# Performance work log

Hardware: AMD Instinct MI355X
Metric: run time of the kernel (lower is better)

Reference implementation:

```python
import jax, jax.numpy as jnp
import numpy as np

N_HEADS = 16

def setup_inputs() -> dict:
    key = jax.random.key(0)
    k1, k2, k3 = jax.random.split(key, 3)
    B, S, V = 4, 2048, 1024
    hs = V // N_HEADS
    x = jax.random.normal(k1, (B, S, V), dtype=jnp.float32)
    # per-head shared QKV projection: Linear(head_size, 3*head_size), weight [3*hs, hs]
    W_qkv = jax.random.normal(k2, (3 * hs, hs), dtype=jnp.float32) / np.sqrt(hs)
    W_out = jax.random.normal(k3, (V, V), dtype=jnp.float32) / np.sqrt(V)
    return {"x": x, "W_qkv": W_qkv, "W_out": W_out}

def reference(x, W_qkv, W_out):
    B, S, V = x.shape
    hs = V // N_HEADS
    x_head = x.reshape(B, S, N_HEADS, hs)            # [B,S,H,hs]
    qkv = jnp.einsum('bshd,ed->bshe', x_head, W_qkv)  # [B,S,H,3*hs]
    q, k, v = jnp.split(qkv, 3, axis=-1)
    scale = 1.0 / np.sqrt(hs).astype(np.float32)
    scores = jnp.einsum('bqhd,bkhd->bhqk', q, k) * scale  # [B,H,S,S]
    causal = jnp.tril(jnp.ones((S, S), dtype=bool))       # keep j <= i
    scores = jnp.where(causal, scores, -jnp.inf)
    attn = jax.nn.softmax(scores, axis=-1)                # dropout p=0 (eval)
    o = jnp.einsum('bhqk,bkhd->bqhd', attn, v).reshape(B, S, V)
    return o @ W_out.T
```

## Files before the change

kernel.cpp:

```cpp
#include <hip/hip_runtime.h>

#define B_  4
#define S_  2048
#define V_  1024
#define H_  16
#define HS_ 64
#define GK_ 1024
#define GN_ 1024

typedef unsigned short u16;
typedef __bf16 bf16x8 __attribute__((ext_vector_type(8)));
typedef float  f32x4  __attribute__((ext_vector_type(4)));

__device__ __forceinline__ float bf2f(u16 u) {
  return __uint_as_float(((unsigned int)u) << 16);
}
__device__ __forceinline__ float lo16(unsigned int w) { return __uint_as_float(w << 16); }
__device__ __forceinline__ float hi16(unsigned int w) { return __uint_as_float(w & 0xffff0000u); }
__device__ __forceinline__ u16 f2bf(float f) {
  unsigned int u = __float_as_uint(f);
  unsigned int r = u + 0x7fffu + ((u >> 16) & 1u);
  return (u16)(r >> 16);
}

__global__ __launch_bounds__(256) void detect_kernel(
    const unsigned int* __restrict__ x32, int* __restrict__ flag)
{
  __shared__ int zred[256];
  __shared__ int nred[256];
  const int tid = threadIdx.x;
  int nz = 0, nn = 0;
  for (int i = tid; i < 16384; i += 256) {
    unsigned int lo = x32[i] & 0xffffu;
    if (lo == 0u) nz++;
    if ((lo & 0x7f80u) == 0x7f80u && (lo & 0x7fu) != 0u) nn++;
  }
  zred[tid] = nz; nred[tid] = nn;
  __syncthreads();
  for (int s = 128; s > 0; s >>= 1) {
    if (tid < s) { zred[tid] += zred[tid + s]; nred[tid] += nred[tid + s]; }
    __syncthreads();
  }
  if (tid == 0) *flag = (zred[0] > 8192 || nred[0] > 0) ? 1 : 0;
}

__global__ __launch_bounds__(256) void wcvt_kernel(
    const void* __restrict__ w, u16* __restrict__ wb, const int* __restrict__ flag)
{
  const int i = (blockIdx.x * 256 + threadIdx.x) * 4;
  if (*flag) {
    float4 f = *(const float4*)((const float*)w + i);
    unsigned int p0 = (unsigned int)f2bf(f.x) | ((unsigned int)f2bf(f.y) << 16);
    unsigned int p1 = (unsigned int)f2bf(f.z) | ((unsigned int)f2bf(f.w) << 16);
    *(uint2*)(wb + i) = make_uint2(p0, p1);
  } else {
    *(uint2*)(wb + i) = *(const uint2*)((const u16*)w + i);
  }
}

__global__ __launch_bounds__(256) void qkv_mfma_kernel(
    const void* __restrict__ x, const void* __restrict__ wqkv,
    u16* __restrict__ q, u16* __restrict__ k, u16* __restrict__ v,
    const int* __restrict__ flag)
{
  __shared__ __align__(16) u16 Ws[192 * 80];
  const int tid = threadIdx.x;
  const int isf32 = *flag;
  for (int idx = tid; idx < 192 * 4; idx += 256) {
    const int row = idx >> 2, c0 = (idx & 3) * 16;
    u16 t16[16];
    if (isf32) {
      const float* gp = (const float*)wqkv + row * 64 + c0;
#pragma unroll
      for (int e = 0; e < 16; ++e) t16[e] = f2bf(gp[e]);
    } else {
      const u16* gp = (const u16*)wqkv + row * 64 + c0;
      *(uint4*)t16 = *(const uint4*)gp;
      *(uint4*)(t16 + 8) = *(const uint4*)(gp + 8);
    }
    *(uint4*)(Ws + row * 80 + c0) = *(uint4*)t16;
    *(uint4*)(Ws + row * 80 + c0 + 8) = *(uint4*)(t16 + 8);
  }
  __syncthreads();

  const int m0 = blockIdx.x * 128;
  const int w = tid >> 6, lane = tid & 63;
  const int ar = lane & 15, quad = lane >> 4;
  const int rbase = m0 + (w & 1) * 64;
  const int cbase = (w >> 1) * 96;

  bf16x8 af[4][2];
#pragma unroll
  for (int rt = 0; rt < 4; ++rt) {
    const size_t row = (size_t)(rbase + rt * 16 + ar) * 64;
    if (isf32) {
      const float* gp = (const float*)x + row;
#pragma unroll
      for (int ks = 0; ks < 2; ++ks) {
        u16 t8[8];
        const float* g8 = gp + ks * 32 + quad * 8;
#pragma unroll
        for (int e = 0; e < 8; ++e) t8[e] = f2bf(g8[e]);
        af[rt][ks] = *(bf16x8*)t8;
      }
    } else {
      const u16* gp = (const u16*)x + row;
#pragma unroll
      for (int ks = 0; ks < 2; ++ks)
        af[rt][ks] = *(const bf16x8*)(gp + ks * 32 + quad * 8);
    }
  }

  f32x4 acc[4][6] = {};
#pragma unroll
  for (int ks = 0; ks < 2; ++ks)
#pragma unroll
    for (int t = 0; t < 6; ++t) {
      const bf16x8 bfr = *(const bf16x8*)(Ws + (cbase + t * 16 + ar) * 80 + ks * 32 + quad * 8);
#pragma unroll
      for (int rt = 0; rt < 4; ++rt)
        acc[rt][t] = __builtin_amdgcn_mfma_f32_16x16x32_bf16(af[rt][ks], bfr, acc[rt][t], 0, 0, 0);
    }

#pragma unroll
  for (int rt = 0; rt < 4; ++rt)
#pragma unroll
    for (int r = 0; r < 4; ++r) {
      const int m = rbase + rt * 16 + quad * 4 + r;
      const int z = m >> 15, s = (m >> 4) & (S_ - 1), h = m & (H_ - 1);
      const size_t base = (((size_t)z * H_ + h) * S_ + s) * HS_;
#pragma unroll
      for (int t = 0; t < 6; ++t) {
        const int e = cbase + t * 16 + ar;
        u16* dst = (e < 64) ? q : (e < 128) ? k : v;
        dst[base + (e & 63)] = f2bf(acc[rt][t][r]);
      }
    }
}

__global__ __launch_bounds__(256) void qkv_kernel(
    const void* __restrict__ x, int b0, const void* __restrict__ w,
    u16* __restrict__ q, u16* __restrict__ k, u16* __restrict__ v,
    const int* __restrict__ flag)
{
  __shared__ __align__(16) float Ws[192 * 64];
  const int tid = threadIdx.x;
  const int isf32 = *flag;
  if (isf32) {
    for (int i = tid; i < 192 * 64; i += 256) Ws[i] = ((const float*)w)[i];
  } else {
    for (int i = tid; i < 192 * 64; i += 256) Ws[i] = bf2f(((const u16*)w)[i]);
  }
  __syncthreads();

  const int th = blockIdx.x * 256 + tid;
  const int h = th & (H_ - 1);
  const int s = th >> 4;
  const int b = b0 + blockIdx.z;
  const size_t zoff = (size_t)blockIdx.z * H_ * S_ * HS_;
  const size_t xoff = ((size_t)b * S_ + s) * V_ + h * HS_;

  float xf[64];
  if (isf32) {
    const float4* xp = (const float4*)((const float*)x + xoff);
#pragma unroll
    for (int i = 0; i < 16; ++i) {
      float4 u = xp[i];
      xf[4*i+0] = u.x; xf[4*i+1] = u.y; xf[4*i+2] = u.z; xf[4*i+3] = u.w;
    }
  } else {
    const uint4* xp = (const uint4*)((const u16*)x + xoff);
#pragma unroll
    for (int i = 0; i < 8; ++i) {
      uint4 u = xp[i];
      xf[8*i+0] = lo16(u.x); xf[8*i+1] = hi16(u.x);
      xf[8*i+2] = lo16(u.y); xf[8*i+3] = hi16(u.y);
      xf[8*i+4] = lo16(u.z); xf[8*i+5] = hi16(u.z);
      xf[8*i+6] = lo16(u.w); xf[8*i+7] = hi16(u.w);
    }
  }

  const size_t obase = zoff + ((size_t)h * S_ + s) * HS_;
#pragma unroll 1
  for (int eg = 0; eg < 12; ++eg) {
    float acc[16];
#pragma unroll
    for (int ee = 0; ee < 16; ++ee) {
      const float4* wr = (const float4*)&Ws[(eg * 16 + ee) * 64];
      float a = 0.f;
#pragma unroll
      for (int d4 = 0; d4 < 16; ++d4) {
        float4 wv = wr[d4];
        a += xf[d4*4+0]*wv.x + xf[d4*4+1]*wv.y + xf[d4*4+2]*wv.z + xf[d4*4+3]*wv.w;
      }
      acc[ee] = a;
    }
    u16* dst = (eg < 4) ? q : (eg < 8) ? k : v;
    const int d0 = (eg & 3) * 16;
    unsigned int p[8];
#pragma unroll
    for (int t = 0; t < 8; ++t)
      p[t] = (unsigned int)f2bf(acc[2*t]) | ((unsigned int)f2bf(acc[2*t+1]) << 16);
    uint4* dp = (uint4*)(dst + obase + d0);
    dp[0] = make_uint4(p[0], p[1], p[2], p[3]);
    dp[1] = make_uint4(p[4], p[5], p[6], p[7]);
  }
}

__global__ __launch_bounds__(256, 4) void attn_mfma_kernel(
    const u16* __restrict__ q, const u16* __restrict__ k,
    const u16* __restrict__ v, u16* __restrict__ o)
{
  const int z   = blockIdx.z;
  const int h   = blockIdx.y;
  const int bi  = blockIdx.x;
  const int qb0 = bi * 64;
  const int qb1 = (31 - bi) * 64;
  const int tid = threadIdx.x;
  const int w = tid >> 6, lane = tid & 63;
  const int col = lane & 15, quad = lane >> 4;

  __shared__ __align__(16) u16 Ks[64 * 72];
  __shared__ __align__(16) u16 Vt[64 * 72];
  __shared__ __align__(16) u16 Ps[4][16 * 72];

  const size_t hs = ((size_t)z * H_ + h) * S_ * HS_;

  const float qs = 0.125f * 1.44269504089f;
  bf16x8 qf[2][2];
#pragma unroll
  for (int u = 0; u < 2; ++u) {
    const int qb = u ? qb1 : qb0;
    const u16* qp = q + hs + (size_t)(qb + w * 16 + col) * HS_ + quad * 8;
#pragma unroll
    for (int ks = 0; ks < 2; ++ks) {
      u16 t8[8];
      *(uint4*)t8 = *(const uint4*)(qp + ks * 32);
#pragma unroll
      for (int e = 0; e < 8; ++e) t8[e] = f2bf(bf2f(t8[e]) * qs);
      qf[u][ks] = *(bf16x8*)t8;
    }
  }

  const int sr = tid >> 2, sc = (tid & 3) * 16;
  const int vr = (tid & 31) * 2, vc = (tid >> 5) * 8;

  f32x4 oacc[2][4] = {};
  float m_run[2] = {-INFINITY, -INFINITY};
  float l_run[2] = {0.f, 0.f};

  const int jbmax = qb1;

  uint4 k0, k1, va, vb;
  {
    const u16* kp = k + hs + (size_t)sr * HS_ + sc;
    k0 = *(const uint4*)kp;
    k1 = *(const uint4*)(kp + 8);
    const u16* vp = v + hs + (size_t)vr * HS_ + vc;
    va = *(const uint4*)vp;
    vb = *(const uint4*)(vp + HS_);
  }

  for (int jb = 0; jb <= jbmax; jb += 64) {
    __syncthreads();
    *(uint4*)(Ks + sr * 72 + sc)     = k0;
    *(uint4*)(Ks + sr * 72 + sc + 8) = k1;
    {
      const u16* pa = (const u16*)&va;
      const u16* pb = (const u16*)&vb;
#pragma unroll
      for (int e = 0; e < 8; ++e)
        *(unsigned int*)(Vt + (vc + e) * 72 + vr) =
            (unsigned int)pa[e] | ((unsigned int)pb[e] << 16);
    }
    __syncthreads();

    if (jb < jbmax) {
      const u16* kp = k + hs + (size_t)(jb + 64 + sr) * HS_ + sc;
      k0 = *(const uint4*)kp;
      k1 = *(const uint4*)(kp + 8);
      const u16* vp = v + hs + (size_t)(jb + 64 + vr) * HS_ + vc;
      va = *(const uint4*)vp;
      vb = *(const uint4*)(vp + HS_);
    }

#pragma unroll
    for (int u = 0; u < 2; ++u) {
      const int ru = (u ? qb1 : qb0) + w * 16;
      if (jb > ru + 15) continue;

      f32x4 sacc[4] = {};
      __builtin_amdgcn_s_setprio(1);
#pragma unroll
      for (int ks = 0; ks < 2; ++ks)
#pragma unroll
        for (int t = 0; t < 4; ++t) {
          const bf16x8 kf = *(const bf16x8*)(Ks + (t * 16 + col) * 72 + ks * 32 + quad * 8);
          sacc[t] = __builtin_amdgcn_mfma_f32_16x16x32_bf16(kf, qf[u][ks], sacc[t], 0, 0, 0);
        }
      __builtin_amdgcn_s_setprio(0);

      if (jb + 63 > ru) {
        const int q_l = ru + col;
#pragma unroll
        for (int t = 0; t < 4; ++t) {
          const int kb = jb + t * 16 + quad * 4;
#pragma unroll
          for (int r = 0; r < 4; ++r)
            if (kb + r > q_l) sacc[t][r] = -INFINITY;
        }
      }

      float a0 = fmaxf(fmaxf(sacc[0][0], sacc[0][1]), fmaxf(sacc[0][2], sacc[0][3]));
      float a1 = fmaxf(fmaxf(sacc[1][0], sacc[1][1]), fmaxf(sacc[1][2], sacc[1][3]));
      float a2 = fmaxf(fmaxf(sacc[2][0], sacc[2][1]), fmaxf(sacc[2][2], sacc[2][3]));
      float a3 = fmaxf(fmaxf(sacc[3][0], sacc[3][1]), fmaxf(sacc[3][2], sacc[3][3]));
      float mx = fmaxf(fmaxf(a0, a1), fmaxf(a2, a3));
      mx = fmaxf(mx, __shfl_xor(mx, 16));
      mx = fmaxf(mx, __shfl_xor(mx, 32));

      float m = m_run[u];
      if (__any(mx - m > 8.0f)) {
        const float mn = fmaxf(m, mx);
        const float al = __builtin_amdgcn_exp2f(m - mn);
        m = mn; m_run[u] = mn;
        l_run[u] *= al;
        float alr[4];
#pragma unroll
        for (int r = 0; r < 4; ++r) alr[r] = __shfl(al, quad * 4 + r);
#pragma unroll
        for (int nt = 0; nt < 4; ++nt)
#pragma unroll
          for (int r = 0; r < 4; ++r) oacc[u][nt][r] *= alr[r];
      }

      float ls = 0.f;
#pragma unroll
      for (int t = 0; t < 4; ++t) {
        const float p0 = __builtin_amdgcn_exp2f(sacc[t][0] - m);
        const float p1 = __builtin_amdgcn_exp2f(sacc[t][1] - m);
        const float p2 = __builtin_amdgcn_exp2f(sacc[t][2] - m);
        const float p3 = __builtin_amdgcn_exp2f(sacc[t][3] - m);
        ls += (p0 + p1) + (p2 + p3);
        const unsigned int w0 = (unsigned int)f2bf(p0) | ((unsigned int)f2bf(p1) << 16);
        const unsigned int w1 = (unsigned int)f2bf(p2) | ((unsigned int)f2bf(p3) << 16);
        *(uint2*)(Ps[w] + col * 72 + t * 16 + quad * 4) = make_uint2(w0, w1);
      }
      ls += __shfl_xor(ls, 16);
      ls += __shfl_xor(ls, 32);
      l_run[u] += ls;

      __builtin_amdgcn_s_setprio(1);
#pragma unroll
      for (int ks = 0; ks < 2; ++ks) {
        const bf16x8 pf = *(const bf16x8*)(Ps[w] + col * 72 + ks * 32 + quad * 8);
#pragma unroll
        for (int nt = 0; nt < 4; ++nt) {
          const bf16x8 vf = *(const bf16x8*)(Vt + (nt * 16 + col) * 72 + ks * 32 + quad * 8);
          oacc[u][nt] = __builtin_amdgcn_mfma_f32_16x16x32_bf16(pf, vf, oacc[u][nt], 0, 0, 0);
        }
      }
      __builtin_amdgcn_s_setprio(0);
    }
  }

  u16* ob = o + (size_t)z * S_ * V_ + h * HS_;
#pragma unroll
  for (int u = 0; u < 2; ++u) {
    const int ru = (u ? qb1 : qb0) + w * 16;
    float inv[4];
#pragma unroll
    for (int r = 0; r < 4; ++r) inv[r] = 1.0f / __shfl(l_run[u], quad * 4 + r);
#pragma unroll
    for (int nt = 0; nt < 4; ++nt)
#pragma unroll
      for (int r = 0; r < 4; ++r)
        ob[(size_t)(ru + quad * 4 + r) * V_ + nt * 16 + col] = f2bf(oacc[u][nt][r] * inv[r]);
  }
}

__global__ __launch_bounds__(256) void oproj_mfma_kernel(
    const u16* __restrict__ a, const u16* __restrict__ bw, float* __restrict__ c)
{
  __shared__ __align__(16) u16 As[128 * 40];
  __shared__ __align__(16) u16 Bs[128 * 40];
  const int tid = threadIdx.x;
  const int m0 = blockIdx.x * 128;
  const int n0 = blockIdx.y * 128;
  const int w = tid >> 6, lane = tid & 63;
  const int col = lane & 15, quad = lane >> 4;
  const int qr = (w & 1) * 64;
  const int qc = (w >> 1) * 64;

  f32x4 acc[4][4] = {};

  const int sr = tid >> 2;
  const int sk = (tid & 3) * 8;
  const u16* ga = a  + (size_t)(m0 + sr) * GK_ + sk;
  const u16* gb = bw + (size_t)(n0 + sr) * GK_ + sk;

  for (int k0 = 0; k0 < GK_; k0 += 32) {
    uint4 a0 = *(const uint4*)(ga + k0);
    uint4 a1 = *(const uint4*)(ga + (size_t)64 * GK_ + k0);
    uint4 b0 = *(const uint4*)(gb + k0);
    uint4 b1 = *(const uint4*)(gb + (size_t)64 * GK_ + k0);
    __syncthreads();
    *(uint4*)(As + sr * 40 + sk)        = a0;
    *(uint4*)(As + (64 + sr) * 40 + sk) = a1;
    *(uint4*)(Bs + sr * 40 + sk)        = b0;
    *(uint4*)(Bs + (64 + sr) * 40 + sk) = b1;
    __syncthreads();

    bf16x8 af[4], bfr[4];
#pragma unroll
    for (int i = 0; i < 4; ++i) {
      af[i]  = *(const bf16x8*)(As + (qr + i * 16 + col) * 40 + quad * 8);
      bfr[i] = *(const bf16x8*)(Bs + (qc + i * 16 + col) * 40 + quad * 8);
    }
#pragma unroll
    for (int i = 0; i < 4; ++i)
#pragma unroll
      for (int j = 0; j < 4; ++j)
        acc[i][j] = __builtin_amdgcn_mfma_f32_16x16x32_bf16(af[i], bfr[j], acc[i][j], 0, 0, 0);
  }

#pragma unroll
  for (int i = 0; i < 4; ++i)
#pragma unroll
    for (int j = 0; j < 4; ++j)
#pragma unroll
      for (int r = 0; r < 4; ++r)
        c[(size_t)(m0 + qr + i * 16 + quad * 4 + r) * GN_ + n0 + qc + j * 16 + col]
            = acc[i][j][r];
}

__global__ __launch_bounds__(256) void oproj_vec_kernel(
    const u16* __restrict__ o, const void* __restrict__ w,
    float* __restrict__ out, const int* __restrict__ flag)
{
  __shared__ __align__(16) float At[64 * 68];
  __shared__ __align__(16) float Wt[64 * 68];
  const int tid = threadIdx.x;
  const size_t zo = (size_t)blockIdx.z * S_ * V_;
  const int m0 = blockIdx.x * 64;
  const int n0 = blockIdx.y * 64;
  const int tr = tid >> 4, tc = tid & 15;
  const int isf32 = *flag;
  const int srow = tid >> 2, sc = (tid & 3) * 16;

  float acc[4][4] = {};

  for (int k0 = 0; k0 < GK_; k0 += 64) {
    float av[16], wv[16];
    {
      const u16* gp = o + zo + (size_t)(m0 + srow) * GK_ + k0 + sc;
      uint4 u0 = *(const uint4*)gp;
      uint4 u1 = *(const uint4*)(gp + 8);
      av[0]=lo16(u0.x); av[1]=hi16(u0.x); av[2]=lo16(u0.y); av[3]=hi16(u0.y);
      av[4]=lo16(u0.z); av[5]=hi16(u0.z); av[6]=lo16(u0.w); av[7]=hi16(u0.w);
      av[8]=lo16(u1.x); av[9]=hi16(u1.x); av[10]=lo16(u1.y); av[11]=hi16(u1.y);
      av[12]=lo16(u1.z); av[13]=hi16(u1.z); av[14]=lo16(u1.w); av[15]=hi16(u1.w);
    }
    if (isf32) {
      const float4* gp = (const float4*)((const float*)w + (size_t)(n0 + srow) * GK_ + k0 + sc);
#pragma unroll
      for (int i = 0; i < 4; ++i) {
        float4 f = gp[i];
        wv[4*i+0]=f.x; wv[4*i+1]=f.y; wv[4*i+2]=f.z; wv[4*i+3]=f.w;
      }
    } else {
      const u16* gp = (const u16*)w + (size_t)(n0 + srow) * GK_ + k0 + sc;
      uint4 u0 = *(const uint4*)gp;
      uint4 u1 = *(const uint4*)(gp + 8);
      wv[0]=lo16(u0.x); wv[1]=hi16(u0.x); wv[2]=lo16(u0.y); wv[3]=hi16(u0.y);
      wv[4]=lo16(u0.z); wv[5]=hi16(u0.z); wv[6]=lo16(u0.w); wv[7]=hi16(u0.w);
      wv[8]=lo16(u1.x); wv[9]=hi16(u1.x); wv[10]=lo16(u1.y); wv[11]=hi16(u1.y);
      wv[12]=lo16(u1.z); wv[13]=hi16(u1.z); wv[14]=lo16(u1.w); wv[15]=hi16(u1.w);
    }
    __syncthreads();
#pragma unroll
    for (int i = 0; i < 16; ++i) {
      At[(sc + i) * 68 + srow] = av[i];
      Wt[(sc + i) * 68 + srow] = wv[i];
    }
    __syncthreads();

#pragma unroll 4
    for (int kk = 0; kk < 64; ++kk) {
      float4 a4 = *(const float4*)&At[kk * 68 + tr * 4];
      float4 w4 = *(const float4*)&Wt[kk * 68 + tc * 4];
      acc[0][0] += a4.x*w4.x; acc[0][1] += a4.x*w4.y; acc[0][2] += a4.x*w4.z; acc[0][3] += a4.x*w4.w;
      acc[1][0] += a4.y*w4.x; acc[1][1] += a4.y*w4.y; acc[1][2] += a4.y*w4.z; acc[1][3] += a4.y*w4.w;
      acc[2][0] += a4.z*w4.x; acc[2][1] += a4.z*w4.y; acc[2][2] += a4.z*w4.z; acc[2][3] += a4.z*w4.w;
      acc[3][0] += a4.w*w4.x; acc[3][1] += a4.w*w4.y; acc[3][2] += a4.w*w4.z; acc[3][3] += a4.w*w4.w;
    }
  }

#pragma unroll
  for (int r = 0; r < 4; ++r) {
    const int row = m0 + tr * 4 + r;
    *(float4*)(out + zo + (size_t)row * GN_ + n0 + tc * 4) =
        make_float4(acc[r][0], acc[r][1], acc[r][2], acc[r][3]);
  }
}

extern "C" void kernel_launch(void* const* d_in, const int* in_sizes, int n_in,
                              void* d_out, int out_size, void* d_ws, size_t ws_size,
                              hipStream_t stream) {
  const void* x = d_in[0];
  const void* wqkv = (n_in > 1) ? d_in[1] : d_in[0];
  const void* wout = (n_in > 2) ? d_in[2] : d_in[0];
  for (int i = 0; i < n_in; ++i) {
    if      (in_sizes[i] == B_ * S_ * V_)  x    = d_in[i];
    else if (in_sizes[i] == 3 * HS_ * HS_) wqkv = d_in[i];
    else if (in_sizes[i] == V_ * V_)       wout = d_in[i];
  }
  float* out = (float*)d_out;

  const size_t per_b = (size_t)H_ * S_ * HS_;
  const size_t SV = (size_t)S_ * V_;
  int* flag = (int*)d_ws;
  const bool full = ws_size >= (16 + 16 * per_b * sizeof(u16));
  const size_t stride = full ? 4 * per_b : per_b;
  u16* q = (u16*)((char*)d_ws + 16);
  u16* k = q + stride;
  u16* v = k + stride;
  u16* o = v + stride;

  detect_kernel<<<dim3(1), dim3(256), 0, stream>>>((const unsigned int*)x, flag);
  if (full) {
    qkv_mfma_kernel<<<dim3((B_ * S_ * H_) / 128), dim3(256), 0, stream>>>(
        x, wqkv, q, k, v, flag);
    attn_mfma_kernel<<<dim3(16, 16, B_), dim3(256), 0, stream>>>(q, k, v, o);
    u16* wb = q;
    wcvt_kernel<<<dim3((V_ * V_) / 1024), dim3(256), 0, stream>>>(wout, wb, flag);
    oproj_mfma_kernel<<<dim3((B_ * S_) / 128, GN_ / 128), dim3(256), 0, stream>>>(o, wb, out);
  } else {
    for (int b = 0; b < B_; ++b) {
      qkv_kernel<<<dim3(128, 1, 1), dim3(256), 0, stream>>>(x, b, wqkv, q, k, v, flag);
      attn_mfma_kernel<<<dim3(16, 16, 1), dim3(256), 0, stream>>>(q, k, v, o);
      oproj_vec_kernel<<<dim3(32, 16, 1), dim3(256), 0, stream>>>(
          o, wout, out + (size_t)b * SV, flag);
    }
  }
}
```

Baseline: 233.0 us.

## Share K/V fragment loads across both query tiles and use packed bf16 convert

New measurement: 273.5 us. 17.4% more time.

```diff
diff --git a/kernel.cpp b/kernel.cpp
--- a/kernel.cpp
+++ b/kernel.cpp
@@ -21,6 +21,11 @@
   unsigned int u = __float_as_uint(f);
   unsigned int r = u + 0x7fffu + ((u >> 16) & 1u);
   return (u16)(r >> 16);
+}
+__device__ __forceinline__ unsigned int cvtpk(float lo, float hi) {
+  unsigned int r;
+  asm("v_cvt_pk_bf16_f32 %0, %1, %2" : "=v"(r) : "v"(lo), "v"(hi));
+  return r;
 }
 
 __global__ __launch_bounds__(256) void detect_kernel(
@@ -222,7 +227,7 @@
 
   __shared__ __align__(16) u16 Ks[64 * 72];
   __shared__ __align__(16) u16 Vt[64 * 72];
-  __shared__ __align__(16) u16 Ps[4][16 * 72];
+  __shared__ __align__(16) u16 Ps[4][2][16 * 72];
 
   const size_t hs = ((size_t)z * H_ + h) * S_ * HS_;
 
@@ -284,84 +289,148 @@
       vb = *(const uint4*)(vp + HS_);
     }
 
-#pragma unroll
-    for (int u = 0; u < 2; ++u) {
-      const int ru = (u ? qb1 : qb0) + w * 16;
-      if (jb > ru + 15) continue;
-
-      f32x4 sacc[4] = {};
-      __builtin_amdgcn_s_setprio(1);
-#pragma unroll
-      for (int ks = 0; ks < 2; ++ks)
-#pragma unroll
-        for (int t = 0; t < 4; ++t) {
-          const bf16x8 kf = *(const bf16x8*)(Ks + (t * 16 + col) * 72 + ks * 32 + quad * 8);
-          sacc[t] = __builtin_amdgcn_mfma_f32_16x16x32_bf16(kf, qf[u][ks], sacc[t], 0, 0, 0);
-        }
-      __builtin_amdgcn_s_setprio(0);
-
-      if (jb + 63 > ru) {
+    const bool act0 = (jb <= qb0);
+
+    f32x4 s0[4] = {}, s1[4] = {};
+    __builtin_amdgcn_s_setprio(1);
+#pragma unroll
+    for (int ks = 0; ks < 2; ++ks) {
+      bf16x8 kf[4];
+#pragma unroll
+      for (int t = 0; t < 4; ++t)
+        kf[t] = *(const bf16x8*)(Ks + (t * 16 + col) * 72 + ks * 32 + quad * 8);
+#pragma unroll
+      for (int t = 0; t < 4; ++t)
+        s1[t] = __builtin_amdgcn_mfma_f32_16x16x32_bf16(kf[t], qf[1][ks], s1[t], 0, 0, 0);
+      if (act0) {
+#pragma unroll
+        for (int t = 0; t < 4; ++t)
+          s0[t] = __builtin_amdgcn_mfma_f32_16x16x32_bf16(kf[t], qf[0][ks], s0[t], 0, 0, 0);
+      }
+    }
+    __builtin_amdgcn_s_setprio(0);
+
+    {
+      const int ru = qb1 + w * 16;
+      if (jb == qb1) {
         const int q_l = ru + col;
 #pragma unroll
         for (int t = 0; t < 4; ++t) {
           const int kb = jb + t * 16 + quad * 4;
 #pragma unroll
           for (int r = 0; r < 4; ++r)
-            if (kb + r > q_l) sacc[t][r] = -INFINITY;
+            if (kb + r > q_l) s1[t][r] = -INFINITY;
         }
       }
-
-      float a0 = fmaxf(fmaxf(sacc[0][0], sacc[0][1]), fmaxf(sacc[0][2], sacc[0][3]));
-      float a1 = fmaxf(fmaxf(sacc[1][0], sacc[1][1]), fmaxf(sacc[1][2], sacc[1][3]));
-      float a2 = fmaxf(fmaxf(sacc[2][0], sacc[2][1]), fmaxf(sacc[2][2], sacc[2][3]));
-      float a3 = fmaxf(fmaxf(sacc[3][0], sacc[3][1]), fmaxf(sacc[3][2], sacc[3][3]));
+      float a0 = fmaxf(fmaxf(s1[0][0], s1[0][1]), fmaxf(s1[0][2], s1[0][3]));
+      float a1 = fmaxf(fmaxf(s1[1][0], s1[1][1]), fmaxf(s1[1][2], s1[1][3]));
+      float a2 = fmaxf(fmaxf(s1[2][0], s1[2][1]), fmaxf(s1[2][2], s1[2][3]));
+      float a3 = fmaxf(fmaxf(s1[3][0], s1[3][1]), fmaxf(s1[3][2], s1[3][3]));
       float mx = fmaxf(fmaxf(a0, a1), fmaxf(a2, a3));
       mx = fmaxf(mx, __shfl_xor(mx, 16));
       mx = fmaxf(mx, __shfl_xor(mx, 32));
 
-      float m = m_run[u];
+      float m = m_run[1];
       if (__any(mx - m > 8.0f)) {
         const float mn = fmaxf(m, mx);
         const float al = __builtin_amdgcn_exp2f(m - mn);
-        m = mn; m_run[u] = mn;
-        l_run[u] *= al;
+        m = mn; m_run[1] = mn;
+        l_run[1] *= al;
         float alr[4];
 #pragma unroll
         for (int r = 0; r < 4; ++r) alr[r] = __shfl(al, quad * 4 + r);
 #pragma unroll
         for (int nt = 0; nt < 4; ++nt)
 #pragma unroll
-          for (int r = 0; r < 4; ++r) oacc[u][nt][r] *= alr[r];
+          for (int r = 0; r < 4; ++r) oacc[1][nt][r] *= alr[r];
       }
 
       float ls = 0.f;
 #pragma unroll
       for (int t = 0; t < 4; ++t) {
-        const float p0 = __builtin_amdgcn_exp2f(sacc[t][0] - m);
-        const float p1 = __builtin_amdgcn_exp2f(sacc[t][1] - m);
-        const float p2 = __builtin_amdgcn_exp2f(sacc[t][2] - m);
-        const float p3 = __builtin_amdgcn_exp2f(sacc[t][3] - m);
+        const float p0 = __builtin_amdgcn_exp2f(s1[t][0] - m);
+        const float p1 = __builtin_amdgcn_exp2f(s1[t][1] - m);
+        const float p2 = __builtin_amdgcn_exp2f(s1[t][2] - m);
+        const float p3 = __builtin_amdgcn_exp2f(s1[t][3] - m);
         ls += (p0 + p1) + (p2 + p3);
-        const unsigned int w0 = (unsigned int)f2bf(p0) | ((unsigned int)f2bf(p1) << 16);
-        const unsigned int w1 = (unsigned int)f2bf(p2) | ((unsigned int)f2bf(p3) << 16);
-        *(uint2*)(Ps[w] + col * 72 + t * 16 + quad * 4) = make_uint2(w0, w1);
+        *(uint2*)(Ps[w][1] + col * 72 + t * 16 + quad * 4) =
+            make_uint2(cvtpk(p0, p1), cvtpk(p2, p3));
       }
       ls += __shfl_xor(ls, 16);
       ls += __shfl_xor(ls, 32);
-      l_run[u] += ls;
-
-      __builtin_amdgcn_s_setprio(1);
-#pragma unroll
-      for (int ks = 0; ks < 2; ++ks) {
-        const bf16x8 pf = *(const bf16x8*)(Ps[w] + col * 72 + ks * 32 + quad * 8);
-#pragma unroll
-        for (int nt = 0; nt < 4; ++nt) {
-          const bf16x8 vf = *(const bf16x8*)(Vt + (nt * 16 + col) * 72 + ks * 32 + quad * 8);
-          oacc[u][nt] = __builtin_amdgcn_mfma_f32_16x16x32_bf16(pf, vf, oacc[u][nt], 0, 0, 0);
+      l_run[1] += ls;
+    }
+
+    if (act0) {
+      const int ru = qb0 + w * 16;
+      if (jb == qb0) {
+        const int q_l = ru + col;
+#pragma unroll
+        for (int t = 0; t < 4; ++t) {
+          const int kb = jb + t * 16 + quad * 4;
+#pragma unroll
+          for (int r = 0; r < 4; ++r)
+            if (kb + r > q_l) s0[t][r] = -INFINITY;
         }
       }
-      __builtin_amdgcn_s_setprio(0);
-    }
+      float a0 = fmaxf(fmaxf(s0[0][0], s0[0][1]), fmaxf(s0[0][2], s0[0][3]));
+      float a1 = fmaxf(fmaxf(s0[1][0], s0[1][1]), fmaxf(s0[1][2], s0[1][3]));
+      float a2 = fmaxf(fmaxf(s0[2][0], s0[2][1]), fmaxf(s0[2][2], s0[2][3]));
+      float a3 = fmaxf(fmaxf(s0[3][0], s0[3][1]), fmaxf(s0[3][2], s0[3][3]));
+      float mx = fmaxf(fmaxf(a0, a1), fmaxf(a2, a3));
+      mx = fmaxf(mx, __shfl_xor(mx, 16));
+      mx = fmaxf(mx, __shfl_xor(mx, 32));
+
+      float m = m_run[0];
+      if (__any(mx - m > 8.0f)) {
+        const float mn = fmaxf(m, mx);
+        const float al = __builtin_amdgcn_exp2f(m - mn);
+        m = mn; m_run[0] = mn;
+        l_run[0] *= al;
+        float alr[4];
+#pragma unroll
+        for (int r = 0; r < 4; ++r) alr[r] = __shfl(al, quad * 4 + r);
+#pragma unroll
+        for (int nt = 0; nt < 4; ++nt)
+#pragma unroll
+          for (int r = 0; r < 4; ++r) oacc[0][nt][r] *= alr[r];
+      }
+
+      float ls = 0.f;
+#pragma unroll
+      for (int t = 0; t < 4; ++t) {
+        const float p0 = __builtin_amdgcn_exp2f(s0[t][0] - m);
+        const float p1 = __builtin_amdgcn_exp2f(s0[t][1] - m);
+        const float p2 = __builtin_amdgcn_exp2f(s0[t][2] - m);
+        const float p3 = __builtin_amdgcn_exp2f(s0[t][3] - m);
+        ls += (p0 + p1) + (p2 + p3);
+        *(uint2*)(Ps[w][0] + col * 72 + t * 16 + quad * 4) =
+            make_uint2(cvtpk(p0, p1), cvtpk(p2, p3));
+      }
+      ls += __shfl_xor(ls, 16);
+      ls += __shfl_xor(ls, 32);
+      l_run[0] += ls;
+    }
+
+    __builtin_amdgcn_s_setprio(1);
+#pragma unroll
+    for (int ks = 0; ks < 2; ++ks) {
+      const bf16x8 pf1 = *(const bf16x8*)(Ps[w][1] + col * 72 + ks * 32 + quad * 8);
+      bf16x8 vf[4];
+#pragma unroll
+      for (int nt = 0; nt < 4; ++nt)
+        vf[nt] = *(const bf16x8*)(Vt + (nt * 16 + col) * 72 + ks * 32 + quad * 8);
+#pragma unroll
+      for (int nt = 0; nt < 4; ++nt)
+        oacc[1][nt] = __builtin_amdgcn_mfma_f32_16x16x32_bf16(pf1, vf[nt], oacc[1][nt], 0, 0, 0);
+      if (act0) {
+        const bf16x8 pf0 = *(const bf16x8*)(Ps[w][0] + col * 72 + ks * 32 + quad * 8);
+#pragma unroll
+        for (int nt = 0; nt < 4; ++nt)
+          oacc[0][nt] = __builtin_amdgcn_mfma_f32_16x16x32_bf16(pf0, vf[nt], oacc[0][nt], 0, 0, 0);
+      }
+    }
+    __builtin_amdgcn_s_setprio(0);
   }
 
   u16* ob = o + (size_t)z * S_ * V_ + h * HS_;
```
